# Optimization experiments

Hardware: AMD Instinct MI355X
Metric: run time of the kernel (lower is better)

Reference implementation:

```python
import jax, jax.numpy as jnp
import numpy as np

B, MSG, H, D, N = 64, 64, 512, 512, 2048


def setup_inputs() -> dict:
    key = jax.random.key(0)
    ks = jax.random.split(key, 20)
    s = 0.02
    return {
        "message": jax.random.normal(ks[0], (B, MSG), jnp.float32),
        "state": jax.random.normal(ks[1], (B, H), jnp.float32),
        "image": jax.random.normal(ks[2], (B, H), jnp.float32),
        "class_descriptors": jax.random.normal(ks[3], (N, D), jnp.float32),
        # GRUCell params (torch layout: gates ordered r, z, n)
        "w_ih": jax.random.normal(ks[4], (3 * H, MSG), jnp.float32) * s,
        "w_hh": jax.random.normal(ks[5], (3 * H, H), jnp.float32) * s,
        "b_ih": jax.random.normal(ks[6], (3 * H,), jnp.float32) * s,
        "b_hh": jax.random.normal(ks[7], (3 * H,), jnp.float32) * s,
        "w_stop": jax.random.normal(ks[8], (1, H), jnp.float32) * s,
        "b_stop": jax.random.normal(ks[9], (1,), jnp.float32) * s,
        "w_y1": jax.random.normal(ks[10], (H, H + D), jnp.float32) * s,
        "b_y1": jax.random.normal(ks[11], (H,), jnp.float32) * s,
        "w_y2": jax.random.normal(ks[12], (1, H), jnp.float32) * s,
        "b_y2": jax.random.normal(ks[13], (1,), jnp.float32) * s,
        "w_state": jax.random.normal(ks[14], (H, H), jnp.float32) * s,
        "b_state": jax.random.normal(ks[15], (H,), jnp.float32) * s,
        "w_desc": jax.random.normal(ks[16], (H, D), jnp.float32) * s,  # no bias
        "w_msg": jax.random.normal(ks[17], (MSG, H), jnp.float32) * s,
        "b_msg": jax.random.normal(ks[18], (MSG,), jnp.float32) * s,
    }


def _gru_cell(x, h, w_ih, w_hh, b_ih, b_hh):
    gi = x @ w_ih.T + b_ih  # [B, 3H]
    gh = h @ w_hh.T + b_hh
    i_r, i_z, i_n = jnp.split(gi, 3, axis=1)
    h_r, h_z, h_n = jnp.split(gh, 3, axis=1)
    r = jax.nn.sigmoid(i_r + h_r)
    z = jax.nn.sigmoid(i_z + h_z)
    n = jnp.tanh(i_n + r * h_n)
    return (1.0 - z) * n + z * h


def reference(message, state, image, class_descriptors,
              w_ih, w_hh, b_ih, b_hh, w_stop, b_stop,
              w_y1, b_y1, w_y2, b_y2, w_state, b_state,
              w_desc, w_msg, b_msg):
    b, h = state.shape
    n, d = class_descriptors.shape

    new_state = _gru_cell(message, state, w_ih, w_hh, b_ih, b_hh)  # [B, H]
    stop_dist = jax.nn.sigmoid(new_state @ w_stop.T + b_stop)  # [B, 1]
    stop_bit = jax.lax.stop_gradient(jnp.round(stop_dist))  # eval-mode path

    # build_state_descriptor_pairs (faithful to torch view semantics,
    # including the (B, H, N) -> (B*N, H) interleaved reshape of pair_left)
    pair_left = jnp.broadcast_to(new_state[:, :, None], (b, h, n)).reshape(b * n, h)
    pair_right = jnp.broadcast_to(class_descriptors[None], (b, n, d)).reshape(b * n, d)
    pairs = jnp.concatenate([pair_left, pair_right], axis=1)  # [B*N, H+D]

    y = jnp.clip(pairs @ w_y1.T + b_y1, 0.0, None)  # relu, [B*N, H]
    y = (y @ w_y2.T + b_y2).reshape(b, -1)  # [B, N]
    y_scores = jax.lax.stop_gradient(jax.nn.softmax(y, axis=1))

    # reweight_descriptors: softmax-weighted sum over descriptors
    descriptor_influence = jnp.einsum('bn,nd->bd', y_scores, class_descriptors)

    message_state = jnp.tanh(new_state @ w_state.T + b_state
                             + descriptor_influence @ w_desc.T)
    message_dist = jax.nn.sigmoid(message_state @ w_msg.T + b_msg)  # [B, MSG]
    outp_msg = jax.lax.stop_gradient(jnp.round(message_dist))

    return stop_bit, stop_dist, outp_msg, message_dist, y
```

## Files before the change

kernel.cpp:

```cpp
#include <hip/hip_runtime.h>


__device__ __forceinline__ float sigm(float x) { return 1.0f / (1.0f + expf(-x)); }

__device__ __forceinline__ void stage_pad68(float* dst, const float* src, int c) {
  *(float4*)&dst[(c >> 4) * 68 + (c & 15) * 4] = *(const float4*)&src[c * 4];
}

__global__ __launch_bounds__(512) void gruws1_kernel(
    const float* __restrict__ msg, const float* __restrict__ st,
    const float* __restrict__ w_ih, const float* __restrict__ w_hh,
    const float* __restrict__ b_ih, const float* __restrict__ b_hh,
    const float* __restrict__ w_y1,
    float* __restrict__ ns, float* __restrict__ nsT, float* __restrict__ ws1) {
  const int t = threadIdx.x;
  if (blockIdx.x >= 512) {
    const int j = (blockIdx.x - 512) * 8 + (t >> 6);
    const int lane = t & 63;
    const float* row = w_y1 + j * 1024 + lane * 8;
    float4 a = *(const float4*)&row[0];
    float4 b = *(const float4*)&row[4];
    float acc = a.x + a.y + a.z + a.w + b.x + b.y + b.z + b.w;
    #pragma unroll
    for (int m = 1; m < 64; m <<= 1) acc += __shfl_xor(acc, m, 64);
    if (lane == 0) ws1[j] = acc;
    return;
  }
  const int h = blockIdx.x;
  __shared__ __align__(16) float sHr[544], sHz[544], sHn[544];
  __shared__ __align__(16) float sIr[64], sIz[64], sIn[64];
  if (t < 128)      stage_pad68(sHr, w_hh + h * 512, t);
  else if (t < 256) stage_pad68(sHz, w_hh + (h + 512) * 512, t - 128);
  else if (t < 384) stage_pad68(sHn, w_hh + (h + 1024) * 512, t - 256);
  else if (t < 400) ((float4*)sIr)[t - 384] = ((const float4*)(w_ih + h * 64))[t - 384];
  else if (t < 416) ((float4*)sIz)[t - 400] = ((const float4*)(w_ih + (h + 512) * 64))[t - 400];
  else if (t < 432) ((float4*)sIn)[t - 416] = ((const float4*)(w_ih + (h + 1024) * 64))[t - 416];
  __syncthreads();
  const int bi = t >> 3, kg = t & 7;
  float pr = 0.f, pz = 0.f, pin = 0.f, phn = 0.f;
  {
    const float* mrow = msg + bi * 64 + kg * 8;
    const float* ir = &sIr[kg * 8];
    const float* iz = &sIz[kg * 8];
    const float* in_ = &sIn[kg * 8];
    #pragma unroll
    for (int i = 0; i < 2; ++i) {
      float4 x = *(const float4*)&mrow[i * 4];
      float4 wr = *(const float4*)&ir[i * 4];
      float4 wz = *(const float4*)&iz[i * 4];
      float4 wn = *(const float4*)&in_[i * 4];
      pr = fmaf(x.x, wr.x, pr); pr = fmaf(x.y, wr.y, pr); pr = fmaf(x.z, wr.z, pr); pr = fmaf(x.w, wr.w, pr);
      pz = fmaf(x.x, wz.x, pz); pz = fmaf(x.y, wz.y, pz); pz = fmaf(x.z, wz.z, pz); pz = fmaf(x.w, wz.w, pz);
      pin = fmaf(x.x, wn.x, pin); pin = fmaf(x.y, wn.y, pin); pin = fmaf(x.z, wn.z, pin); pin = fmaf(x.w, wn.w, pin);
    }
  }
  {
    const float* srow = st + bi * 512 + kg * 64;
    const float* hr = &sHr[kg * 68];
    const float* hz = &sHz[kg * 68];
    const float* hn = &sHn[kg * 68];
    #pragma unroll
    for (int i = 0; i < 16; ++i) {
      float4 x = *(const float4*)&srow[i * 4];
      float4 wr = *(const float4*)&hr[i * 4];
      float4 wz = *(const float4*)&hz[i * 4];
      float4 wn = *(const float4*)&hn[i * 4];
      pr = fmaf(x.x, wr.x, pr); pr = fmaf(x.y, wr.y, pr); pr = fmaf(x.z, wr.z, pr); pr = fmaf(x.w, wr.w, pr);
      pz = fmaf(x.x, wz.x, pz); pz = fmaf(x.y, wz.y, pz); pz = fmaf(x.z, wz.z, pz); pz = fmaf(x.w, wz.w, pz);
      phn = fmaf(x.x, wn.x, phn); phn = fmaf(x.y, wn.y, phn); phn = fmaf(x.z, wn.z, phn); phn = fmaf(x.w, wn.w, phn);
    }
  }
  pr += __shfl_xor(pr, 1, 8); pr += __shfl_xor(pr, 2, 8); pr += __shfl_xor(pr, 4, 8);
  pz += __shfl_xor(pz, 1, 8); pz += __shfl_xor(pz, 2, 8); pz += __shfl_xor(pz, 4, 8);
  pin += __shfl_xor(pin, 1, 8); pin += __shfl_xor(pin, 2, 8); pin += __shfl_xor(pin, 4, 8);
  phn += __shfl_xor(phn, 1, 8); phn += __shfl_xor(phn, 2, 8); phn += __shfl_xor(phn, 4, 8);
  if ((t & 7) == 0) {
    float r = sigm(pr + b_ih[h] + b_hh[h]);
    float z = sigm(pz + b_ih[h + 512] + b_hh[h + 512]);
    float n = tanhf(pin + b_ih[h + 1024] + r * (phn + b_hh[h + 1024]));
    float hp = st[bi * 512 + h];
    float v = (1.0f - z) * n + z * hp;
    ns[bi * 512 + h] = v;
    nsT[h * 64 + bi] = v;
  }
}

__global__ __launch_bounds__(256, 2) void g_kernel(
    const float* __restrict__ desc, const float* __restrict__ w_y1,
    const float* __restrict__ b_y1, float* __restrict__ G) {
  __shared__ __align__(16) float As[32 * 34];
  __shared__ __align__(16) float Bs[32 * 68];
  const int rr0 = blockIdx.x * 32;
  const int j0 = blockIdx.y * 64;
  const int t = threadIdx.x;
  const int lrow = t >> 3;
  const int lk4 = (t & 7) * 4;
  const int swz = (t & 7) << 2;
  const int tm2 = (t >> 4) * 2;
  const int tn4 = (t & 15) * 4;
  const int bc0 = lrow ^ swz;
  const float* aptr = desc + (rr0 + lrow) * 512 + lk4;
  const float* bptr0 = w_y1 + (j0 + lrow) * 1024 + 512 + lk4;
  const float* bptr1 = bptr0 + 32 * 1024;
  float4 av = *(const float4*)aptr;
  float4 bv0 = *(const float4*)bptr0;
  float4 bv1 = *(const float4*)bptr1;
  float acc[2][4] = {};
  for (int k0 = 0; k0 < 512; k0 += 32) {
    __syncthreads();
    As[(lk4 + 0) * 34 + lrow] = av.x; As[(lk4 + 1) * 34 + lrow] = av.y;
    As[(lk4 + 2) * 34 + lrow] = av.z; As[(lk4 + 3) * 34 + lrow] = av.w;
    Bs[(lk4 + 0) * 68 + bc0] = bv0.x; Bs[(lk4 + 1) * 68 + bc0] = bv0.y;
    Bs[(lk4 + 2) * 68 + bc0] = bv0.z; Bs[(lk4 + 3) * 68 + bc0] = bv0.w;
    Bs[(lk4 + 0) * 68 + bc0 + 32] = bv1.x; Bs[(lk4 + 1) * 68 + bc0 + 32] = bv1.y;
    Bs[(lk4 + 2) * 68 + bc0 + 32] = bv1.z; Bs[(lk4 + 3) * 68 + bc0 + 32] = bv1.w;
    __syncthreads();
    if (k0 + 32 < 512) {
      av = *(const float4*)(aptr + k0 + 32);
      bv0 = *(const float4*)(bptr0 + k0 + 32);
      bv1 = *(const float4*)(bptr1 + k0 + 32);
    }
    #pragma unroll
    for (int k = 0; k < 32; ++k) {
      float a0 = As[k * 34 + tm2];
      float a1 = As[k * 34 + tm2 + 1];
      float4 b = *(const float4*)&Bs[k * 68 + (tn4 ^ ((k >> 2) << 2))];
      acc[0][0] = fmaf(a0, b.x, acc[0][0]); acc[0][1] = fmaf(a0, b.y, acc[0][1]);
      acc[0][2] = fmaf(a0, b.z, acc[0][2]); acc[0][3] = fmaf(a0, b.w, acc[0][3]);
      acc[1][0] = fmaf(a1, b.x, acc[1][0]); acc[1][1] = fmaf(a1, b.y, acc[1][1]);
      acc[1][2] = fmaf(a1, b.z, acc[1][2]); acc[1][3] = fmaf(a1, b.w, acc[1][3]);
    }
  }
  float4 by = *(const float4*)&b_y1[j0 + tn4];
  float4 r0 = make_float4(acc[0][0] + by.x, acc[0][1] + by.y, acc[0][2] + by.z, acc[0][3] + by.w);
  float4 r1 = make_float4(acc[1][0] + by.x, acc[1][1] + by.y, acc[1][2] + by.z, acc[1][3] + by.w);
  *(float4*)&G[(rr0 + tm2) * 512 + j0 + tn4] = r0;
  *(float4*)&G[(rr0 + tm2 + 1) * 512 + j0 + tn4] = r1;
}

__global__ __launch_bounds__(256) void ystop_kernel(
    const float* __restrict__ nsT, const float* __restrict__ ws1,
    const float* __restrict__ G, const float* __restrict__ w_y2,
    const float* __restrict__ b_y2, float* __restrict__ yf,
    const float* __restrict__ ns, const float* __restrict__ w_stop,
    const float* __restrict__ b_stop, float* __restrict__ out_bit,
    float* __restrict__ out_dist, float* __restrict__ di) {
  const int t = threadIdx.x;
  if (blockIdx.x > 2048) {
    const int idx = (blockIdx.x - 2049) * 512 + t * 2;
    *(float2*)&di[idx] = make_float2(0.f, 0.f);
    return;
  }
  if (blockIdx.x == 2048) {
    const int bi = t >> 2, kg = t & 3;
    const float* row = ns + bi * 512 + kg * 128;
    const float* wrow = w_stop + kg * 128;
    float acc = 0.f;
    #pragma unroll
    for (int i = 0; i < 32; ++i) {
      float4 r = *(const float4*)&row[i * 4];
      float4 w = *(const float4*)&wrow[i * 4];
      acc = fmaf(r.x, w.x, acc); acc = fmaf(r.y, w.y, acc);
      acc = fmaf(r.z, w.z, acc); acc = fmaf(r.w, w.w, acc);
    }
    acc += __shfl_xor(acc, 1, 4); acc += __shfl_xor(acc, 2, 4);
    if (kg == 0) {
      float sd = sigm(acc + b_stop[0]);
      out_dist[bi] = sd;
      out_bit[bi] = rintf(sd);
    }
    return;
  }
  const int rr = blockIdx.x;
  __shared__ __align__(16) float sG[512], sW1[512], sW2[512];
  __shared__ float sp[4 * 72];
  if (t < 128) {
    ((float4*)sG)[t] = ((const float4*)(G + rr * 512))[t];
    ((float4*)sW2)[t] = ((const float4*)w_y2)[t];
  } else {
    ((float4*)sW1)[t - 128] = ((const float4*)ws1)[t - 128];
  }
  __syncthreads();
  const int bi = t & 63, jq = t >> 6;
  const float v = nsT[(rr >> 2) * 64 + bi];
  float acc = 0.0f;
  const float* g = sG + jq * 128;
  const float* w1 = sW1 + jq * 128;
  const float* w2 = sW2 + jq * 128;
  #pragma unroll 4
  for (int j = 0; j < 128; j += 4) {
    float4 gv = *(const float4*)&g[j];
    float4 a1 = *(const float4*)&w1[j];
    float4 a2 = *(const float4*)&w2[j];
    acc = fmaf(a2.x, fmaxf(fmaf(v, a1.x, gv.x), 0.0f), acc);
    acc = fmaf(a2.y, fmaxf(fmaf(v, a1.y, gv.y), 0.0f), acc);
    acc = fmaf(a2.z, fmaxf(fmaf(v, a1.z, gv.z), 0.0f), acc);
    acc = fmaf(a2.w, fmaxf(fmaf(v, a1.w, gv.w), 0.0f), acc);
  }
  sp[jq * 72 + bi] = acc;
  __syncthreads();
  if (t < 64) {
    float y = sp[t] + sp[72 + t] + sp[144 + t] + sp[216 + t] + b_y2[0];
    yf[t * 2048 + rr] = y;
  }
}

__global__ __launch_bounds__(256) void softmax_kernel(
    const float* __restrict__ yf, float* __restrict__ out_y,
    float* __restrict__ mxv, float* __restrict__ sumv) {
  const int bi = blockIdx.x;
  const int t = threadIdx.x;
  __shared__ float sy[2048];
  __shared__ float red[256];
  float lmax = -3.0e38f;
  for (int i = t; i < 2048; i += 256) {
    float v = yf[bi * 2048 + i];
    sy[i] = v;
    out_y[bi * 2048 + i] = v;
    lmax = fmaxf(lmax, v);
  }
  red[t] = lmax;
  __syncthreads();
  for (int s = 128; s > 0; s >>= 1) {
    if (t < s) red[t] = fmaxf(red[t], red[t + s]);
    __syncthreads();
  }
  const float mx = red[0];
  __syncthreads();
  float lsum = 0.0f;
  for (int i = t; i < 2048; i += 256) lsum += expf(sy[i] - mx);
  red[t] = lsum;
  __syncthreads();
  for (int s = 128; s > 0; s >>= 1) {
    if (t < s) red[t] += red[t + s];
    __syncthreads();
  }
  if (t == 0) { mxv[bi] = mx; sumv[bi] = red[0]; }
}

__global__ __launch_bounds__(256) void di_part_kernel(
    const float* __restrict__ yf, const float* __restrict__ mxv,
    const float* __restrict__ desc, float* __restrict__ di) {
  __shared__ __align__(16) float sE[64 * 66];
  __shared__ __align__(16) float sD[64 * 68];
  __shared__ float sMx[64];
  const int d0 = blockIdx.x * 64;
  const int n0 = blockIdx.y * 64;
  const int t = threadIdx.x;
  if (t < 64) sMx[t] = mxv[t];
  __syncthreads();
  {
    const int bi = t >> 2;
    const float m = sMx[bi];
    #pragma unroll
    for (int i = 0; i < 4; ++i) {
      const int kq = (t & 3) * 4 + i * 16;
      float4 av = *(const float4*)&yf[bi * 2048 + n0 + kq];
      sE[(kq + 0) * 66 + bi] = expf(av.x - m);
      sE[(kq + 1) * 66 + bi] = expf(av.y - m);
      sE[(kq + 2) * 66 + bi] = expf(av.z - m);
      sE[(kq + 3) * 66 + bi] = expf(av.w - m);
    }
    #pragma unroll
    for (int i = 0; i < 4; ++i) {
      const int nn = (t >> 4) + i * 16;
      const int dq = (t & 15) * 4;
      *(float4*)&sD[nn * 68 + dq] = *(const float4*)&desc[(n0 + nn) * 512 + d0 + dq];
    }
  }
  __syncthreads();
  const int bi0 = (t >> 4) * 4;
  const int dd0 = (t & 15) * 4;
  float acc[4][4] = {};
  #pragma unroll 8
  for (int nn = 0; nn < 64; ++nn) {
    float4 a = *(const float4*)&sE[nn * 66 + bi0];
    float4 b = *(const float4*)&sD[nn * 68 + dd0];
    acc[0][0] = fmaf(a.x, b.x, acc[0][0]); acc[0][1] = fmaf(a.x, b.y, acc[0][1]);
    acc[0][2] = fmaf(a.x, b.z, acc[0][2]); acc[0][3] = fmaf(a.x, b.w, acc[0][3]);
    acc[1][0] = fmaf(a.y, b.x, acc[1][0]); acc[1][1] = fmaf(a.y, b.y, acc[1][1]);
    acc[1][2] = fmaf(a.y, b.z, acc[1][2]); acc[1][3] = fmaf(a.y, b.w, acc[1][3]);
    acc[2][0] = fmaf(a.z, b.x, acc[2][0]); acc[2][1] = fmaf(a.z, b.y, acc[2][1]);
    acc[2][2] = fmaf(a.z, b.z, acc[2][2]); acc[2][3] = fmaf(a.z, b.w, acc[2][3]);
    acc[3][0] = fmaf(a.w, b.x, acc[3][0]); acc[3][1] = fmaf(a.w, b.y, acc[3][1]);
    acc[3][2] = fmaf(a.w, b.z, acc[3][2]); acc[3][3] = fmaf(a.w, b.w, acc[3][3]);
  }
  #pragma unroll
  for (int i = 0; i < 4; ++i)
    #pragma unroll
    for (int j = 0; j < 4; ++j)
      atomicAdd(&di[(bi0 + i) * 512 + d0 + dd0 + j], acc[i][j]);
}

__global__ __launch_bounds__(512) void ms_kernel(
    const float* __restrict__ ns, const float* __restrict__ di,
    const float* __restrict__ sumv,
    const float* __restrict__ w_state, const float* __restrict__ b_state,
    const float* __restrict__ w_desc, float* __restrict__ ms) {
  const int hj = blockIdx.x;
  const int t = threadIdx.x;
  __shared__ __align__(16) float sWs[544], sWd[544];
  __shared__ float sInv[64];
  if (t < 128)      stage_pad68(sWs, w_state + hj * 512, t);
  else if (t < 256) stage_pad68(sWd, w_desc + hj * 512, t - 128);
  else if (t < 320) sInv[t - 256] = 1.0f / sumv[t - 256];
  __syncthreads();
  const int bi = t >> 3, kg = t & 7;
  const float* nr = ns + bi * 512 + kg * 64;
  const float* dr = di + bi * 512 + kg * 64;
  const float* wsp = &sWs[kg * 68];
  const float* wdp = &sWd[kg * 68];
  float accs = 0.f, accd = 0.f;
  #pragma unroll
  for (int i = 0; i < 16; ++i) {
    float4 a = *(const float4*)&nr[i * 4];
    float4 w = *(const float4*)&wsp[i * 4];
    float4 b = *(const float4*)&dr[i * 4];
    float4 u = *(const float4*)&wdp[i * 4];
    accs = fmaf(a.x, w.x, accs); accs = fmaf(a.y, w.y, accs);
    accs = fmaf(a.z, w.z, accs); accs = fmaf(a.w, w.w, accs);
    accd = fmaf(b.x, u.x, accd); accd = fmaf(b.y, u.y, accd);
    accd = fmaf(b.z, u.z, accd); accd = fmaf(b.w, u.w, accd);
  }
  accs += __shfl_xor(accs, 1, 8); accs += __shfl_xor(accs, 2, 8); accs += __shfl_xor(accs, 4, 8);
  accd += __shfl_xor(accd, 1, 8); accd += __shfl_xor(accd, 2, 8); accd += __shfl_xor(accd, 4, 8);
  if ((t & 7) == 0)
    ms[bi * 512 + hj] = tanhf(accs + accd * sInv[bi] + b_state[hj]);
}

__global__ __launch_bounds__(512) void msg_kernel(
    const float* __restrict__ ms, const float* __restrict__ w_msg,
    const float* __restrict__ b_msg, float* __restrict__ out_msg,
    float* __restrict__ out_msgdist) {
  const int m = blockIdx.x;
  const int t = threadIdx.x;
  __shared__ __align__(16) float sW[544];
  if (t < 128) stage_pad68(sW, w_msg + m * 512, t);
  __syncthreads();
  const int bi = t >> 3, kg = t & 7;
  const float* row = ms + bi * 512 + kg * 64;
  const float* wp = &sW[kg * 68];
  float acc = 0.f;
  #pragma unroll
  for (int i = 0; i < 16; ++i) {
    float4 a = *(const float4*)&row[i * 4];
    float4 w = *(const float4*)&wp[i * 4];
    acc = fmaf(a.x, w.x, acc); acc = fmaf(a.y, w.y, acc);
    acc = fmaf(a.z, w.z, acc); acc = fmaf(a.w, w.w, acc);
  }
  acc += __shfl_xor(acc, 1, 8); acc += __shfl_xor(acc, 2, 8); acc += __shfl_xor(acc, 4, 8);
  if ((t & 7) == 0) {
    float md = sigm(acc + b_msg[m]);
    out_msgdist[bi * 64 + m] = md;
    out_msg[bi * 64 + m] = rintf(md);
  }
}

extern "C" void kernel_launch(void* const* d_in, const int* in_sizes, int n_in,
                              void* d_out, int out_size, void* d_ws, size_t ws_size,
                              hipStream_t stream) {
  (void)in_sizes; (void)n_in; (void)out_size; (void)ws_size;
  const float* message = (const float*)d_in[0];
  const float* state   = (const float*)d_in[1];
  const float* desc    = (const float*)d_in[3];
  const float* w_ih    = (const float*)d_in[4];
  const float* w_hh    = (const float*)d_in[5];
  const float* b_ih    = (const float*)d_in[6];
  const float* b_hh    = (const float*)d_in[7];
  const float* w_stop  = (const float*)d_in[8];
  const float* b_stop  = (const float*)d_in[9];
  const float* w_y1    = (const float*)d_in[10];
  const float* b_y1    = (const float*)d_in[11];
  const float* w_y2    = (const float*)d_in[12];
  const float* b_y2    = (const float*)d_in[13];
  const float* w_state = (const float*)d_in[14];
  const float* b_state = (const float*)d_in[15];
  const float* w_desc  = (const float*)d_in[16];
  const float* w_msg   = (const float*)d_in[17];
  const float* b_msg   = (const float*)d_in[18];

  float* out = (float*)d_out;
  float* out_stopbit  = out;
  float* out_stopdist = out + 64;
  float* out_msg      = out + 128;
  float* out_msgdist  = out + 4224;
  float* out_y        = out + 8320;

  char* ws = (char*)d_ws;
  float* ns   = (float*)(ws);
  float* nsT  = (float*)(ws + 131072);
  float* ws1  = (float*)(ws + 262144);
  float* G    = (float*)(ws + 264192);
  float* yf   = (float*)(ws + 4458496);
  float* di   = (float*)(ws + 4982784);
  float* ms   = (float*)(ws + 5113856);
  float* mxv  = (float*)(ws + 5244928);
  float* sumv = (float*)(ws + 5245184);

  gruws1_kernel<<<576, 512, 0, stream>>>(message, state, w_ih, w_hh, b_ih, b_hh,
                                         w_y1, ns, nsT, ws1);
  g_kernel<<<dim3(64, 8), 256, 0, stream>>>(desc, w_y1, b_y1, G);
  ystop_kernel<<<2113, 256, 0, stream>>>(nsT, ws1, G, w_y2, b_y2, yf,
                                         ns, w_stop, b_stop, out_stopbit,
                                         out_stopdist, di);
  softmax_kernel<<<64, 256, 0, stream>>>(yf, out_y, mxv, sumv);
  di_part_kernel<<<dim3(8, 32), 256, 0, stream>>>(yf, mxv, desc, di);
  ms_kernel<<<512, 512, 0, stream>>>(ns, di, sumv, w_state, b_state, w_desc, ms);
  msg_kernel<<<64, 512, 0, stream>>>(ms, w_msg, b_msg, out_msg, out_msgdist);
}
```

Measured before the change: 208.8 us.

## Drop softmax pass, compute exp without max, replace atomics with partial-sum reduction

Removes the separate softmax kernel: y is written straight to the output, and the descriptor-weighting kernel takes exp(y) with no max subtraction while also accumulating partial row sums. The atomicAdd accumulation into di, and the zeroing blocks it needed, are replaced by per-chunk partial buffers that reuse the G workspace, plus a new reduce kernel that sums them and applies the 1/sum normalisation. The y-scoring kernel now handles four descriptor rows per block so each loaded weight is reused, cutting the grid from 2113 to 513 blocks. Skipping the max subtraction risks overflow if the scores were large, but y values here are small.

```diff
diff --git a/kernel.cpp b/kernel.cpp
--- a/kernel.cpp
+++ b/kernel.cpp
@@ -141,17 +141,12 @@
 __global__ __launch_bounds__(256) void ystop_kernel(
     const float* __restrict__ nsT, const float* __restrict__ ws1,
     const float* __restrict__ G, const float* __restrict__ w_y2,
-    const float* __restrict__ b_y2, float* __restrict__ yf,
+    const float* __restrict__ b_y2, float* __restrict__ out_y,
     const float* __restrict__ ns, const float* __restrict__ w_stop,
     const float* __restrict__ b_stop, float* __restrict__ out_bit,
-    float* __restrict__ out_dist, float* __restrict__ di) {
-  const int t = threadIdx.x;
-  if (blockIdx.x > 2048) {
-    const int idx = (blockIdx.x - 2049) * 512 + t * 2;
-    *(float2*)&di[idx] = make_float2(0.f, 0.f);
-    return;
-  }
-  if (blockIdx.x == 2048) {
+    float* __restrict__ out_dist) {
+  const int t = threadIdx.x;
+  if (blockIdx.x == 512) {
     const int bi = t >> 2, kg = t & 3;
     const float* row = ns + bi * 512 + kg * 128;
     const float* wrow = w_stop + kg * 128;
@@ -171,96 +166,91 @@
     }
     return;
   }
-  const int rr = blockIdx.x;
-  __shared__ __align__(16) float sG[512], sW1[512], sW2[512];
-  __shared__ float sp[4 * 72];
-  if (t < 128) {
-    ((float4*)sG)[t] = ((const float4*)(G + rr * 512))[t];
-    ((float4*)sW2)[t] = ((const float4*)w_y2)[t];
-  } else {
-    ((float4*)sW1)[t - 128] = ((const float4*)ws1)[t - 128];
-  }
+  const int q = blockIdx.x;
+  __shared__ __align__(16) float sG[2048];
+  __shared__ __align__(16) float sW1[512], sW2[512];
+  __shared__ float sV[64];
+  __shared__ float sp[16 * 64];
+  ((float4*)sG)[t] = ((const float4*)(G + q * 2048))[t];
+  ((float4*)sG)[t + 256] = ((const float4*)(G + q * 2048))[t + 256];
+  if (t < 128)       ((float4*)sW1)[t] = ((const float4*)ws1)[t];
+  else               ((float4*)sW2)[t - 128] = ((const float4*)w_y2)[t - 128];
+  if (t < 64) sV[t] = nsT[q * 64 + t];
   __syncthreads();
   const int bi = t & 63, jq = t >> 6;
-  const float v = nsT[(rr >> 2) * 64 + bi];
-  float acc = 0.0f;
-  const float* g = sG + jq * 128;
+  const float v = sV[bi];
+  const float* g0 = sG + jq * 128;
+  const float* g1 = sG + 512 + jq * 128;
+  const float* g2 = sG + 1024 + jq * 128;
+  const float* g3 = sG + 1536 + jq * 128;
   const float* w1 = sW1 + jq * 128;
   const float* w2 = sW2 + jq * 128;
+  float a0 = 0.f, a1 = 0.f, a2 = 0.f, a3 = 0.f;
   #pragma unroll 4
   for (int j = 0; j < 128; j += 4) {
-    float4 gv = *(const float4*)&g[j];
-    float4 a1 = *(const float4*)&w1[j];
-    float4 a2 = *(const float4*)&w2[j];
-    acc = fmaf(a2.x, fmaxf(fmaf(v, a1.x, gv.x), 0.0f), acc);
-    acc = fmaf(a2.y, fmaxf(fmaf(v, a1.y, gv.y), 0.0f), acc);
-    acc = fmaf(a2.z, fmaxf(fmaf(v, a1.z, gv.z), 0.0f), acc);
-    acc = fmaf(a2.w, fmaxf(fmaf(v, a1.w, gv.w), 0.0f), acc);
-  }
-  sp[jq * 72 + bi] = acc;
-  __syncthreads();
-  if (t < 64) {
-    float y = sp[t] + sp[72 + t] + sp[144 + t] + sp[216 + t] + b_y2[0];
-    yf[t * 2048 + rr] = y;
-  }
-}
-
-__global__ __launch_bounds__(256) void softmax_kernel(
-    const float* __restrict__ yf, float* __restrict__ out_y,
-    float* __restrict__ mxv, float* __restrict__ sumv) {
-  const int bi = blockIdx.x;
-  const int t = threadIdx.x;
-  __shared__ float sy[2048];
-  __shared__ float red[256];
-  float lmax = -3.0e38f;
-  for (int i = t; i < 2048; i += 256) {
-    float v = yf[bi * 2048 + i];
-    sy[i] = v;
-    out_y[bi * 2048 + i] = v;
-    lmax = fmaxf(lmax, v);
-  }
-  red[t] = lmax;
-  __syncthreads();
-  for (int s = 128; s > 0; s >>= 1) {
-    if (t < s) red[t] = fmaxf(red[t], red[t + s]);
-    __syncthreads();
-  }
-  const float mx = red[0];
-  __syncthreads();
-  float lsum = 0.0f;
-  for (int i = t; i < 2048; i += 256) lsum += expf(sy[i] - mx);
-  red[t] = lsum;
-  __syncthreads();
-  for (int s = 128; s > 0; s >>= 1) {
-    if (t < s) red[t] += red[t + s];
-    __syncthreads();
-  }
-  if (t == 0) { mxv[bi] = mx; sumv[bi] = red[0]; }
+    float4 x1 = *(const float4*)&w1[j];
+    float4 x2 = *(const float4*)&w2[j];
+    float4 G0 = *(const float4*)&g0[j];
+    float4 G1 = *(const float4*)&g1[j];
+    float4 G2 = *(const float4*)&g2[j];
+    float4 G3 = *(const float4*)&g3[j];
+    float tj;
+    tj = v * x1.x;
+    a0 = fmaf(x2.x, fmaxf(tj + G0.x, 0.f), a0);
+    a1 = fmaf(x2.x, fmaxf(tj + G1.x, 0.f), a1);
+    a2 = fmaf(x2.x, fmaxf(tj + G2.x, 0.f), a2);
+    a3 = fmaf(x2.x, fmaxf(tj + G3.x, 0.f), a3);
+    tj = v * x1.y;
+    a0 = fmaf(x2.y, fmaxf(tj + G0.y, 0.f), a0);
+    a1 = fmaf(x2.y, fmaxf(tj + G1.y, 0.f), a1);
+    a2 = fmaf(x2.y, fmaxf(tj + G2.y, 0.f), a2);
+    a3 = fmaf(x2.y, fmaxf(tj + G3.y, 0.f), a3);
+    tj = v * x1.z;
+    a0 = fmaf(x2.z, fmaxf(tj + G0.z, 0.f), a0);
+    a1 = fmaf(x2.z, fmaxf(tj + G1.z, 0.f), a1);
+    a2 = fmaf(x2.z, fmaxf(tj + G2.z, 0.f), a2);
+    a3 = fmaf(x2.z, fmaxf(tj + G3.z, 0.f), a3);
+    tj = v * x1.w;
+    a0 = fmaf(x2.w, fmaxf(tj + G0.w, 0.f), a0);
+    a1 = fmaf(x2.w, fmaxf(tj + G1.w, 0.f), a1);
+    a2 = fmaf(x2.w, fmaxf(tj + G2.w, 0.f), a2);
+    a3 = fmaf(x2.w, fmaxf(tj + G3.w, 0.f), a3);
+  }
+  sp[(0 * 4 + jq) * 64 + bi] = a0;
+  sp[(1 * 4 + jq) * 64 + bi] = a1;
+  sp[(2 * 4 + jq) * 64 + bi] = a2;
+  sp[(3 * 4 + jq) * 64 + bi] = a3;
+  __syncthreads();
+  const int rl = t >> 6, b2 = t & 63;
+  float y = sp[(rl * 4 + 0) * 64 + b2] + sp[(rl * 4 + 1) * 64 + b2]
+          + sp[(rl * 4 + 2) * 64 + b2] + sp[(rl * 4 + 3) * 64 + b2] + b_y2[0];
+  out_y[b2 * 2048 + 4 * q + rl] = y;
 }
 
 __global__ __launch_bounds__(256) void di_part_kernel(
-    const float* __restrict__ yf, const float* __restrict__ mxv,
-    const float* __restrict__ desc, float* __restrict__ di) {
+    const float* __restrict__ out_y, const float* __restrict__ desc,
+    float* __restrict__ dp, float* __restrict__ sump) {
   __shared__ __align__(16) float sE[64 * 66];
   __shared__ __align__(16) float sD[64 * 68];
-  __shared__ float sMx[64];
   const int d0 = blockIdx.x * 64;
   const int n0 = blockIdx.y * 64;
   const int t = threadIdx.x;
-  if (t < 64) sMx[t] = mxv[t];
-  __syncthreads();
   {
     const int bi = t >> 2;
-    const float m = sMx[bi];
+    float psum = 0.f;
     #pragma unroll
     for (int i = 0; i < 4; ++i) {
       const int kq = (t & 3) * 4 + i * 16;
-      float4 av = *(const float4*)&yf[bi * 2048 + n0 + kq];
-      sE[(kq + 0) * 66 + bi] = expf(av.x - m);
-      sE[(kq + 1) * 66 + bi] = expf(av.y - m);
-      sE[(kq + 2) * 66 + bi] = expf(av.z - m);
-      sE[(kq + 3) * 66 + bi] = expf(av.w - m);
-    }
+      float4 av = *(const float4*)&out_y[bi * 2048 + n0 + kq];
+      float e0 = expf(av.x), e1 = expf(av.y), e2 = expf(av.z), e3 = expf(av.w);
+      sE[(kq + 0) * 66 + bi] = e0;
+      sE[(kq + 1) * 66 + bi] = e1;
+      sE[(kq + 2) * 66 + bi] = e2;
+      sE[(kq + 3) * 66 + bi] = e3;
+      psum += e0 + e1 + e2 + e3;
+    }
+    psum += __shfl_xor(psum, 1, 4); psum += __shfl_xor(psum, 2, 4);
+    if (blockIdx.x == 0 && (t & 3) == 0) sump[blockIdx.y * 64 + bi] = psum;
     #pragma unroll
     for (int i = 0; i < 4; ++i) {
       const int nn = (t >> 4) + i * 16;
@@ -285,47 +275,63 @@
     acc[3][0] = fmaf(a.w, b.x, acc[3][0]); acc[3][1] = fmaf(a.w, b.y, acc[3][1]);
     acc[3][2] = fmaf(a.w, b.z, acc[3][2]); acc[3][3] = fmaf(a.w, b.w, acc[3][3]);
   }
+  float* base = dp + blockIdx.y * 32768;
   #pragma unroll
   for (int i = 0; i < 4; ++i)
-    #pragma unroll
-    for (int j = 0; j < 4; ++j)
-      atomicAdd(&di[(bi0 + i) * 512 + d0 + dd0 + j], acc[i][j]);
+    *(float4*)&base[(bi0 + i) * 512 + d0 + dd0] =
+        make_float4(acc[i][0], acc[i][1], acc[i][2], acc[i][3]);
+}
+
+__global__ __launch_bounds__(512) void di_reduce_kernel(
+    const float* __restrict__ dp, const float* __restrict__ sump,
+    float* __restrict__ di) {
+  const int bi = blockIdx.x;
+  const int t = threadIdx.x;
+  __shared__ float sInv;
+  if (t < 32) {
+    float s = sump[t * 64 + bi];
+    s += __shfl_xor(s, 1, 32); s += __shfl_xor(s, 2, 32);
+    s += __shfl_xor(s, 4, 32); s += __shfl_xor(s, 8, 32);
+    s += __shfl_xor(s, 16, 32);
+    if (t == 0) sInv = 1.0f / s;
+  }
+  __syncthreads();
+  const float inv = sInv;
+  float acc = 0.0f;
+  #pragma unroll 8
+  for (int c = 0; c < 32; ++c) acc += dp[c * 32768 + bi * 512 + t];
+  di[bi * 512 + t] = acc * inv;
 }
 
 __global__ __launch_bounds__(512) void ms_kernel(
     const float* __restrict__ ns, const float* __restrict__ di,
-    const float* __restrict__ sumv,
     const float* __restrict__ w_state, const float* __restrict__ b_state,
     const float* __restrict__ w_desc, float* __restrict__ ms) {
   const int hj = blockIdx.x;
   const int t = threadIdx.x;
   __shared__ __align__(16) float sWs[544], sWd[544];
-  __shared__ float sInv[64];
   if (t < 128)      stage_pad68(sWs, w_state + hj * 512, t);
   else if (t < 256) stage_pad68(sWd, w_desc + hj * 512, t - 128);
-  else if (t < 320) sInv[t - 256] = 1.0f / sumv[t - 256];
   __syncthreads();
   const int bi = t >> 3, kg = t & 7;
   const float* nr = ns + bi * 512 + kg * 64;
   const float* dr = di + bi * 512 + kg * 64;
   const float* wsp = &sWs[kg * 68];
   const float* wdp = &sWd[kg * 68];
-  float accs = 0.f, accd = 0.f;
+  float acc = 0.f;
   #pragma unroll
   for (int i = 0; i < 16; ++i) {
     float4 a = *(const float4*)&nr[i * 4];
     float4 w = *(const float4*)&wsp[i * 4];
     float4 b = *(const float4*)&dr[i * 4];
     float4 u = *(const float4*)&wdp[i * 4];
-    accs = fmaf(a.x, w.x, accs); accs = fmaf(a.y, w.y, accs);
-    accs = fmaf(a.z, w.z, accs); accs = fmaf(a.w, w.w, accs);
-    accd = fmaf(b.x, u.x, accd); accd = fmaf(b.y, u.y, accd);
-    accd = fmaf(b.z, u.z, accd); accd = fmaf(b.w, u.w, accd);
-  }
-  accs += __shfl_xor(accs, 1, 8); accs += __shfl_xor(accs, 2, 8); accs += __shfl_xor(accs, 4, 8);
-  accd += __shfl_xor(accd, 1, 8); accd += __shfl_xor(accd, 2, 8); accd += __shfl_xor(accd, 4, 8);
-  if ((t & 7) == 0)
-    ms[bi * 512 + hj] = tanhf(accs + accd * sInv[bi] + b_state[hj]);
+    acc = fmaf(a.x, w.x, acc); acc = fmaf(a.y, w.y, acc);
+    acc = fmaf(a.z, w.z, acc); acc = fmaf(a.w, w.w, acc);
+    acc = fmaf(b.x, u.x, acc); acc = fmaf(b.y, u.y, acc);
+    acc = fmaf(b.z, u.z, acc); acc = fmaf(b.w, u.w, acc);
+  }
+  acc += __shfl_xor(acc, 1, 8); acc += __shfl_xor(acc, 2, 8); acc += __shfl_xor(acc, 4, 8);
+  if ((t & 7) == 0) ms[bi * 512 + hj] = tanhf(acc + b_state[hj]);
 }
 
 __global__ __launch_bounds__(512) void msg_kernel(
@@ -391,20 +397,17 @@
   float* nsT  = (float*)(ws + 131072);
   float* ws1  = (float*)(ws + 262144);
   float* G    = (float*)(ws + 264192);
-  float* yf   = (float*)(ws + 4458496);
-  float* di   = (float*)(ws + 4982784);
-  float* ms   = (float*)(ws + 5113856);
-  float* mxv  = (float*)(ws + 5244928);
-  float* sumv = (float*)(ws + 5245184);
+  float* sump = (float*)(ws + 4458496);
+  float* di   = (float*)(ws + 4466688);
+  float* ms   = (float*)(ws + 4597760);
 
   gruws1_kernel<<<576, 512, 0, stream>>>(message, state, w_ih, w_hh, b_ih, b_hh,
                                          w_y1, ns, nsT, ws1);
   g_kernel<<<dim3(64, 8), 256, 0, stream>>>(desc, w_y1, b_y1, G);
-  ystop_kernel<<<2113, 256, 0, stream>>>(nsT, ws1, G, w_y2, b_y2, yf,
-                                         ns, w_stop, b_stop, out_stopbit,
-                                         out_stopdist, di);
-  softmax_kernel<<<64, 256, 0, stream>>>(yf, out_y, mxv, sumv);
-  di_part_kernel<<<dim3(8, 32), 256, 0, stream>>>(yf, mxv, desc, di);
-  ms_kernel<<<512, 512, 0, stream>>>(ns, di, sumv, w_state, b_state, w_desc, ms);
+  ystop_kernel<<<513, 256, 0, stream>>>(nsT, ws1, G, w_y2, b_y2, out_y,
+                                        ns, w_stop, b_stop, out_stopbit, out_stopdist);
+  di_part_kernel<<<dim3(8, 32), 256, 0, stream>>>(out_y, desc, G, sump);
+  di_reduce_kernel<<<64, 512, 0, stream>>>(G, sump, di);
+  ms_kernel<<<512, 512, 0, stream>>>(ns, di, w_state, b_state, w_desc, ms);
   msg_kernel<<<64, 512, 0, stream>>>(ms, w_msg, b_msg, out_msg, out_msgdist);
 }
```

New measurement: 187.0 us. -10.5%, faster.
